# Optimization experiments

Measured on AMD Instinct MI355X. Metric: run time of the kernel, lower is better.

The kernel has to match this reference:

```python
import jax, jax.numpy as jnp
import numpy as np

N_NODES = 100000
N_EDGES = 1600000
N_PAIRS = 500000
IN_C, HID_C, OUT_C = 128, 128, 128


def setup_inputs() -> dict:
    key = jax.random.key(0)
    ks = jax.random.split(key, 12)
    def lin(k, fan_in, shape):
        b = 1.0 / np.sqrt(fan_in)
        return jax.random.uniform(k, shape, jnp.float32, -b, b)
    return {
        "x": jax.random.normal(ks[0], (N_NODES, IN_C), jnp.float32),
        "edge_index": jax.random.randint(ks[1], (2, N_EDGES), 0, N_NODES),
        "edge_pairs": jax.random.randint(ks[2], (2, N_PAIRS), 0, N_NODES),
        "W1": lin(ks[3], IN_C, (IN_C, HID_C)),
        "b1": jnp.zeros((HID_C,), jnp.float32),
        "W2": lin(ks[4], HID_C, (HID_C, OUT_C)),
        "b2": jnp.zeros((OUT_C,), jnp.float32),
        "Wm1": lin(ks[5], 2 * OUT_C, (2 * OUT_C, HID_C)),
        "bm1": lin(ks[6], 2 * OUT_C, (HID_C,)),
        "Wm2": lin(ks[7], HID_C, (HID_C, 1)),
        "bm2": lin(ks[8], HID_C, (1,)),
    }


def reference(x, edge_index, edge_pairs, W1, b1, W2, b2, Wm1, bm1, Wm2, bm2):
    N = x.shape[0]
    loop = jnp.arange(N, dtype=edge_index.dtype)
    row = jnp.concatenate([edge_index[0], loop])  # source nodes (+self loops)
    col = jnp.concatenate([edge_index[1], loop])  # target nodes (+self loops)
    # symmetric GCN normalization: deg^{-1/2}[row] * deg^{-1/2}[col]
    deg = jax.ops.segment_sum(jnp.ones(col.shape, x.dtype), col, num_segments=N)
    dinv = jnp.where(deg > 0, jax.lax.rsqrt(deg), 0.0)
    norm = dinv[row] * dinv[col]  # [E+N]

    def gcn_conv(h, W, b):
        h = h @ W  # transform first (PyG GCNConv lin has no bias)
        msg = h[row] * norm[:, None]
        return jax.ops.segment_sum(msg, col, num_segments=N) + b

    h = jax.nn.relu(gcn_conv(x, W1, b1))
    h = gcn_conv(h, W2, b2)  # dropout p=0.0 -> identity

    src, dst = edge_pairs[0], edge_pairs[1]
    ef = jnp.concatenate([h[src], h[dst]], axis=-1)  # [P, 2*out]
    out = jax.nn.relu(ef @ Wm1 + bm1) @ Wm2 + bm2
    return out.squeeze(-1)
```

## Files before the change

### kernel.cpp

```cpp
#include <hip/hip_runtime.h>
#include <hip/hip_fp16.h>

#define NCH 128
#define G_NODES 256
#define EPB 4096
#define RCAP 4864
#define MAXNB 512
#define KST 40

typedef __attribute__((ext_vector_type(8))) short short8;
typedef _Float16 half8 __attribute__((ext_vector_type(8)));
typedef __attribute__((ext_vector_type(4))) float floatx4;

static inline size_t align256(size_t x){ return (x + 255) & ~(size_t)255; }

__global__ __launch_bounds__(256) void wprep2_kernel(
    const float* __restrict__ W2, const float* __restrict__ Wm1,
    const float* __restrict__ b2, const float* __restrict__ bm1,
    short* __restrict__ planes, float* __restrict__ bm1p, float* __restrict__ zbias){
  int b = blockIdx.x, t = threadIdx.x;
  if (b == 128){
    if (t < 128){
      float acc = bm1[t];
      for (int j = 0; j < 128; j++)
        acc += b2[j] * (Wm1[j * 128 + t] + Wm1[(128 + j) * 128 + t]);
      bm1p[t] = acc;
      zbias[t] = 0.f;
    }
    return;
  }
  __shared__ float w2row[128];
  if (t < 128) w2row[t] = W2[b * 128 + t];
  __syncthreads();
  int mat = t >> 7, n = t & 127;
  const float* Wsrc = Wm1 + (size_t)mat * 16384;
  float acc = 0.f;
  #pragma unroll 4
  for (int j = 0; j < 128; j++) acc = fmaf(w2row[j], Wsrc[j * 128 + n], acc);
  __half h = __float2half(acc);
  __half l = __float2half(acc - __half2float(h));
  planes[(size_t)(4 + 2 * mat) * 16384 + n * 128 + b] = __half_as_short(h);
  planes[(size_t)(5 + 2 * mat) * 16384 + n * 128 + b] = __half_as_short(l);
}

__global__ __launch_bounds__(256) void binA_kernel(
    const int* __restrict__ row, const int* __restrict__ col,
    int* __restrict__ gcur, unsigned* __restrict__ bucketed, int E, int NB,
    const float* __restrict__ W1, short* __restrict__ planes){
  __shared__ int cnt[MAXNB];
  __shared__ int lbase[MAXNB];
  __shared__ int gbase[MAXNB];
  __shared__ unsigned sorted[EPB];
  __shared__ unsigned short binOf[EPB];
  __shared__ int sh[256];
  __shared__ int carry;
  int t = threadIdx.x;
  int e0 = blockIdx.x * EPB;
  int ecnt = min(EPB, E - e0);
  for (int i = t; i < NB; i += 256) cnt[i] = 0;
  if (t == 0) carry = 0;
  __syncthreads();
  unsigned rec[16]; int bn[16]; int rk[16];
  #pragma unroll
  for (int i = 0; i < 16; i++){
    int e = e0 + i * 256 + t;
    if (e < E){
      int r = row[e], c = col[e];
      bn[i]  = c >> 8;
      rec[i] = (unsigned)r | ((unsigned)(c & 255) << 17);
      rk[i]  = atomicAdd(&cnt[bn[i]], 1);
    } else bn[i] = -1;
  }
  __syncthreads();
  for (int start = 0; start < NB; start += 256){
    int i = start + t;
    int v = (i < NB) ? cnt[i] : 0;
    sh[t] = v; __syncthreads();
    for (int off = 1; off < 256; off <<= 1){
      int val = (t >= off) ? sh[t - off] : 0;
      __syncthreads(); sh[t] += val; __syncthreads();
    }
    if (i < NB) lbase[i] = sh[t] - v + carry;
    __syncthreads();
    if (t == 255) carry += sh[255];
    __syncthreads();
  }
  for (int i = t; i < NB; i += 256){
    int c = cnt[i];
    gbase[i] = (c > 0) ? atomicAdd(&gcur[i], c) : 0;
  }
  __syncthreads();
  #pragma unroll
  for (int i = 0; i < 16; i++){
    if (bn[i] >= 0){
      int pos = lbase[bn[i]] + rk[i];
      sorted[pos] = rec[i];
      binOf[pos]  = (unsigned short)bn[i];
    }
  }
  __syncthreads();
  for (int idx = t; idx < ecnt; idx += 256){
    int b = binOf[idx];
    int gpos = gbase[b] + (idx - lbase[b]);
    if (gpos < RCAP) bucketed[(size_t)b * RCAP + gpos] = sorted[idx];
  }
  {
    int gid = blockIdx.x * 256 + t;
    if (gid < 16384){
      int k = gid >> 7, n = gid & 127;
      float x = W1[gid];
      unsigned u = __float_as_uint(x);
      short hs = (short)(u >> 16);
      float hf = __uint_as_float(u & 0xFFFF0000u);
      short ls = (short)(__float_as_uint(x - hf) >> 16);
      planes[n * 128 + k]         = hs;
      planes[16384 + n * 128 + k] = ls;
    }
  }
}

__global__ __launch_bounds__(512, 4) void fused_gemm_binB(
    const float* __restrict__ X, const short* __restrict__ Whi_,
    const short* __restrict__ Wlo_, __half* __restrict__ O, int nrows, int gemmBlocks,
    const unsigned* __restrict__ bucketed, const int* __restrict__ gcur,
    int* __restrict__ rows_sorted, int* __restrict__ offs,
    int* __restrict__ counts, float* __restrict__ dinv, int N){
  __shared__ __align__(16) char smem[40960];
  int t = threadIdx.x;
  if (blockIdx.x < gemmBlocks){
    short* Xhi = (short*)smem;
    short* Xlo = Xhi + 128 * KST;
    short* Whi = Xlo + 128 * KST;
    short* Wlo = Whi + 128 * KST;
    int w = t >> 6, lane = t & 63;
    int m = lane & 15, q = lane >> 4;
    int row0 = blockIdx.x * 128;
    floatx4 acc[8];
    #pragma unroll
    for (int ct = 0; ct < 8; ct++) acc[ct] = (floatx4)0.f;
    for (int kc = 0; kc < 4; kc++){
      int k0 = kc * 32;
      __syncthreads();
      #pragma unroll
      for (int qq = 0; qq < 2; qq++){
        int f = t + 512 * qq;
        int r = f >> 3, kq = f & 7;
        int gr = row0 + r;
        int grc = (gr < nrows) ? gr : 0;
        float4 v = *(const float4*)(X + (size_t)grc * NCH + k0 + kq * 4);
        short h[4], l[4];
        float vv[4] = {v.x, v.y, v.z, v.w};
        #pragma unroll
        for (int j = 0; j < 4; j++){
          unsigned u = __float_as_uint(vv[j]);
          h[j] = (short)(u >> 16);
          float hf = __uint_as_float(u & 0xFFFF0000u);
          l[j] = (short)(__float_as_uint(vv[j] - hf) >> 16);
        }
        *(uint2*)(Xhi + r * KST + kq * 4) = *(uint2*)h;
        *(uint2*)(Xlo + r * KST + kq * 4) = *(uint2*)l;
      }
      {
        int n = t >> 2, kq = t & 3;
        *(uint4*)(Whi + n * KST + kq * 8) = *(const uint4*)(Whi_ + n * NCH + k0 + kq * 8);
        *(uint4*)(Wlo + n * KST + kq * 8) = *(const uint4*)(Wlo_ + n * NCH + k0 + kq * 8);
      }
      __syncthreads();
      short8 a_hi = *(const short8*)(Xhi + (w * 16 + m) * KST + q * 8);
      short8 a_lo = *(const short8*)(Xlo + (w * 16 + m) * KST + q * 8);
      #pragma unroll
      for (int ct = 0; ct < 8; ct++){
        short8 b_hi = *(const short8*)(Whi + (ct * 16 + m) * KST + q * 8);
        short8 b_lo = *(const short8*)(Wlo + (ct * 16 + m) * KST + q * 8);
        acc[ct] = __builtin_amdgcn_mfma_f32_16x16x32_bf16(a_hi, b_hi, acc[ct], 0, 0, 0);
        acc[ct] = __builtin_amdgcn_mfma_f32_16x16x32_bf16(a_lo, b_hi, acc[ct], 0, 0, 0);
        acc[ct] = __builtin_amdgcn_mfma_f32_16x16x32_bf16(a_hi, b_lo, acc[ct], 0, 0, 0);
      }
    }
    #pragma unroll
    for (int r = 0; r < 4; r++){
      int grow = row0 + w * 16 + q * 4 + r;
      if (grow < nrows){
        #pragma unroll
        for (int ct = 0; ct < 8; ct++)
          O[(size_t)grow * NCH + ct * 16 + m] = __float2half(acc[ct][r]);
      }
    }
  } else {
    int b = blockIdx.x - gemmBlocks;
    unsigned* ledge = (unsigned*)smem;
    int* cnt  = (int*)(smem + RCAP * 4);
    int* cnt2 = cnt + 256;
    int* lex  = cnt2 + 256;
    int* sh   = lex + 256;
    int size = min(gcur[b], RCAP);
    int n0 = b * G_NODES;
    if (t < 256){ cnt[t] = 0; cnt2[t] = 0; }
    __syncthreads();
    for (int i = t; i < size; i += 512){
      unsigned v = bucketed[(size_t)b * RCAP + i];
      ledge[i] = v;
      atomicAdd(&cnt[v >> 17], 1);
    }
    __syncthreads();
    {
      int v = (t < 256) ? cnt[t] : 0;
      if (t < 256) sh[t] = v;
      __syncthreads();
      for (int off = 1; off < 256; off <<= 1){
        int val = (t >= off && t < 256) ? sh[t - off] : 0;
        __syncthreads();
        if (t < 256) sh[t] += val;
        __syncthreads();
      }
      if (t < 256){
        lex[t] = sh[t] - v;
        int n = n0 + t;
        if (n < N){
          counts[n] = v;
          offs[n]   = b * RCAP + sh[t] - v;
          dinv[n]   = rsqrtf((float)v + 1.0f);
        }
      }
    }
    __syncthreads();
    for (int i = t; i < size; i += 512){
      unsigned v = ledge[i];
      int node = v >> 17;
      int pos = lex[node] + atomicAdd(&cnt2[node], 1);
      rows_sorted[(size_t)b * RCAP + pos] = (int)(v & 0x1FFFFu);
    }
  }
}

template<int NCT>
__global__ __launch_bounds__(512, 4) void gemm_f16k(
    const __half* __restrict__ X,
    const short* __restrict__ Whi0, const short* __restrict__ Wlo0,
    const short* __restrict__ Whi1, const short* __restrict__ Wlo1,
    const float* __restrict__ scale, int do_scale,
    __half* __restrict__ O0, __half* __restrict__ O1, int nrows){
  __shared__ short Xs[128 * KST];
  __shared__ short Whs[NCT * 16 * KST];
  __shared__ short Wls[NCT * 16 * KST];
  int t = threadIdx.x;
  int w = t >> 6, lane = t & 63;
  int m = lane & 15, q = lane >> 4;
  int row0 = blockIdx.x * 128;
  floatx4 acc[NCT];
  #pragma unroll
  for (int ct = 0; ct < NCT; ct++) acc[ct] = (floatx4)0.f;

  for (int kc = 0; kc < 4; kc++){
    int k0 = kc * 32;
    __syncthreads();
    {
      int r = t >> 2, kq = t & 3;
      int gr = row0 + r;
      int grc = (gr < nrows) ? gr : 0;
      *(uint4*)(Xs + r * KST + kq * 8) = *(const uint4*)(X + (size_t)grc * NCH + k0 + kq * 8);
    }
    #pragma unroll
    for (int i = t; i < NCT * 16 * 4; i += 512){
      int n = i >> 2, kq = i & 3;
      const short* sh = (n < 128) ? (Whi0 + n * NCH) : (Whi1 + (n - 128) * NCH);
      const short* sl = (n < 128) ? (Wlo0 + n * NCH) : (Wlo1 + (n - 128) * NCH);
      *(uint4*)(Whs + n * KST + kq * 8) = *(const uint4*)(sh + k0 + kq * 8);
      *(uint4*)(Wls + n * KST + kq * 8) = *(const uint4*)(sl + k0 + kq * 8);
    }
    __syncthreads();
    half8 a = *(const half8*)(Xs + (w * 16 + m) * KST + q * 8);
    #pragma unroll
    for (int ct = 0; ct < NCT; ct++){
      half8 bh = *(const half8*)(Whs + (ct * 16 + m) * KST + q * 8);
      half8 bl = *(const half8*)(Wls + (ct * 16 + m) * KST + q * 8);
      acc[ct] = __builtin_amdgcn_mfma_f32_16x16x32_f16(a, bh, acc[ct], 0, 0, 0);
      acc[ct] = __builtin_amdgcn_mfma_f32_16x16x32_f16(a, bl, acc[ct], 0, 0, 0);
    }
  }
  #pragma unroll
  for (int r = 0; r < 4; r++){
    int grow = row0 + w * 16 + q * 4 + r;
    if (grow < nrows){
      float sc = do_scale ? scale[grow] : 1.0f;
      #pragma unroll
      for (int ct = 0; ct < NCT; ct++){
        __half val = __float2half(acc[ct][r] * sc);
        if (ct < 8) O0[(size_t)grow * NCH + ct * 16 + m] = val;
        else        O1[(size_t)grow * NCH + (ct - 8) * 16 + m] = val;
      }
    }
  }
}

__global__ __launch_bounds__(256) void agg_kernel(
    const __half* __restrict__ s, const float* __restrict__ dinv,
    const int* __restrict__ offs, const int* __restrict__ counts,
    const int* __restrict__ rows_sorted, const float* __restrict__ bias,
    __half* __restrict__ outp, int N, int do_relu, int edge_dinv){
  int wave = (int)((blockIdx.x * blockDim.x + threadIdx.x) >> 6);
  int lane = threadIdx.x & 63;
  if (wave >= N) return;
  int c = wave;
  int g = lane >> 4, h = lane & 15;
  float di = dinv[c];
  float wself = edge_dinv ? di : 1.0f;
  float acc[8] = {0.f,0.f,0.f,0.f,0.f,0.f,0.f,0.f};
  if (g == 0){
    uint4 v = *(const uint4*)(s + (size_t)c * NCH + h * 8);
    const __half2* hp = (const __half2*)&v;
    #pragma unroll
    for (int i = 0; i < 4; i++){
      float2 f = __half22float2(hp[i]);
      acc[2*i] = fmaf(wself, f.x, acc[2*i]); acc[2*i+1] = fmaf(wself, f.y, acc[2*i+1]);
    }
  }
  int off = offs[c], cnt = counts[c];
  for (int chunk = 0; chunk < cnt; chunk += 64){
    int nn = min(64, cnt - chunk);
    int myidx = (lane < nn) ? rows_sorted[off + chunk + lane] : 0;
    float mydinv = 1.0f;
    if (edge_dinv && lane < nn) mydinv = dinv[myidx];
    int jmax = (nn + 3) >> 2;
    #pragma unroll 8
    for (int j = 0; j < jmax; j++){
      int e = 4 * j + g;
      int r  = __shfl(myidx, e & 63, 64);
      float dr = edge_dinv ? __shfl(mydinv, e & 63, 64) : 1.0f;
      if (e < nn){
        uint4 v = *(const uint4*)(s + (size_t)r * NCH + h * 8);
        const __half2* hp = (const __half2*)&v;
        #pragma unroll
        for (int i = 0; i < 4; i++){
          float2 f = __half22float2(hp[i]);
          acc[2*i] = fmaf(dr, f.x, acc[2*i]); acc[2*i+1] = fmaf(dr, f.y, acc[2*i+1]);
        }
      }
    }
  }
  #pragma unroll
  for (int i = 0; i < 8; i++){
    acc[i] += __shfl_xor(acc[i], 16, 64);
    acc[i] += __shfl_xor(acc[i], 32, 64);
  }
  if (g == 0){
    float4 b0 = *(const float4*)(bias + h * 8);
    float4 b1 = *(const float4*)(bias + h * 8 + 4);
    float o[8];
    o[0] = di*acc[0]+b0.x; o[1] = di*acc[1]+b0.y; o[2] = di*acc[2]+b0.z; o[3] = di*acc[3]+b0.w;
    o[4] = di*acc[4]+b1.x; o[5] = di*acc[5]+b1.y; o[6] = di*acc[6]+b1.z; o[7] = di*acc[7]+b1.w;
    if (do_relu){
      #pragma unroll
      for (int i = 0; i < 8; i++) o[i] = fmaxf(o[i], 0.f);
    }
    __half2 packed[4];
    #pragma unroll
    for (int i = 0; i < 4; i++) packed[i] = __floats2half2_rn(o[2*i], o[2*i+1]);
    *(uint4*)(outp + (size_t)c * NCH + h * 8) = *(uint4*)packed;
  }
}

__global__ __launch_bounds__(256) void pair_kernel(
    const __half* __restrict__ A, const __half* __restrict__ B,
    const int* __restrict__ src, const int* __restrict__ dst,
    const float* __restrict__ bm1, const float* __restrict__ Wm2,
    const float* __restrict__ bm2, float* __restrict__ outp, int P){
  int gwave = (int)((blockIdx.x * blockDim.x + threadIdx.x) >> 6);
  int lane  = threadIdx.x & 63;
  int nw    = (int)((gridDim.x * blockDim.x) >> 6);
  int g = lane >> 4, h = lane & 15;
  float bb[8], ww[8];
  {
    float4 t0 = *(const float4*)(bm1 + h * 8);
    float4 t1 = *(const float4*)(bm1 + h * 8 + 4);
    bb[0]=t0.x; bb[1]=t0.y; bb[2]=t0.z; bb[3]=t0.w;
    bb[4]=t1.x; bb[5]=t1.y; bb[6]=t1.z; bb[7]=t1.w;
    float4 w0 = *(const float4*)(Wm2 + h * 8);
    float4 w1 = *(const float4*)(Wm2 + h * 8 + 4);
    ww[0]=w0.x; ww[1]=w0.y; ww[2]=w0.z; ww[3]=w0.w;
    ww[4]=w1.x; ww[5]=w1.y; ww[6]=w1.z; ww[7]=w1.w;
  }
  float bsc = bm2[0];
  const __half* basep = (g & 1) ? B : A;
  const int* idxp = (g & 1) ? dst : src;
  for (int p0 = gwave * 8; p0 < P; p0 += nw * 8){
    int piA = p0 + (g >> 1);
    int piB = p0 + 2 + (g >> 1);
    int piC = p0 + 4 + (g >> 1);
    int piD = p0 + 6 + (g >> 1);
    int piAX = (piA < P) ? piA : P - 1;
    int piBX = (piB < P) ? piB : P - 1;
    int piCX = (piC < P) ? piC : P - 1;
    int piDX = (piD < P) ? piD : P - 1;
    int nodeA = idxp[piAX];
    int nodeB = idxp[piBX];
    int nodeC = idxp[piCX];
    int nodeD = idxp[piDX];
    uint4 vA = *(const uint4*)(basep + (size_t)nodeA * NCH + h * 8);
    uint4 vB = *(const uint4*)(basep + (size_t)nodeB * NCH + h * 8);
    uint4 vC = *(const uint4*)(basep + (size_t)nodeC * NCH + h * 8);
    uint4 vD = *(const uint4*)(basep + (size_t)nodeD * NCH + h * 8);
    const __half2* hpA = (const __half2*)&vA;
    const __half2* hpB = (const __half2*)&vB;
    const __half2* hpC = (const __half2*)&vC;
    const __half2* hpD = (const __half2*)&vD;
    float fA[8], fB[8], fC[8], fD[8];
    #pragma unroll
    for (int i = 0; i < 4; i++){
      float2 ta = __half22float2(hpA[i]);
      float2 tb = __half22float2(hpB[i]);
      float2 tc = __half22float2(hpC[i]);
      float2 td = __half22float2(hpD[i]);
      fA[2*i] = ta.x; fA[2*i+1] = ta.y;
      fB[2*i] = tb.x; fB[2*i+1] = tb.y;
      fC[2*i] = tc.x; fC[2*i+1] = tc.y;
      fD[2*i] = td.x; fD[2*i+1] = td.y;
    }
    float pA = 0.f, pB = 0.f, pC = 0.f, pD = 0.f;
    #pragma unroll
    for (int i = 0; i < 8; i++){
      float oA = __shfl_xor(fA[i], 16, 64);
      float oB = __shfl_xor(fB[i], 16, 64);
      float oC = __shfl_xor(fC[i], 16, 64);
      float oD = __shfl_xor(fD[i], 16, 64);
      float zA = fmaxf(fA[i] + oA + bb[i], 0.f);
      float zB = fmaxf(fB[i] + oB + bb[i], 0.f);
      float zC = fmaxf(fC[i] + oC + bb[i], 0.f);
      float zD = fmaxf(fD[i] + oD + bb[i], 0.f);
      pA += zA * ww[i];
      pB += zB * ww[i];
      pC += zC * ww[i];
      pD += zD * ww[i];
    }
    #pragma unroll
    for (int d = 1; d <= 8; d <<= 1){
      pA += __shfl_xor(pA, d, 64);
      pB += __shfl_xor(pB, d, 64);
      pC += __shfl_xor(pC, d, 64);
      pD += __shfl_xor(pD, d, 64);
    }
    if ((lane & 31) == 0){
      if (piA < P) outp[piA] = pA + bsc;
      if (piB < P) outp[piB] = pB + bsc;
      if (piC < P) outp[piC] = pC + bsc;
      if (piD < P) outp[piD] = pD + bsc;
    }
  }
}


extern "C" void kernel_launch(void* const* d_in, const int* in_sizes, int n_in,
                              void* d_out, int out_size, void* d_ws, size_t ws_size,
                              hipStream_t stream){
  const float* x   = (const float*)d_in[0];
  const int*   ei  = (const int*)  d_in[1];
  const int*   ep  = (const int*)  d_in[2];
  const float* W1  = (const float*)d_in[3];
  const float* b1  = (const float*)d_in[4];
  const float* W2  = (const float*)d_in[5];
  const float* b2  = (const float*)d_in[6];
  const float* Wm1 = (const float*)d_in[7];
  const float* bm1 = (const float*)d_in[8];
  const float* Wm2 = (const float*)d_in[9];
  const float* bm2 = (const float*)d_in[10];
  float* outp = (float*)d_out;

  const int N = in_sizes[0] / NCH;
  const int E = in_sizes[1] / 2;
  const int P = in_sizes[2] / 2;
  const int NB = (N + G_NODES - 1) / G_NODES;

  char* base = (char*)d_ws;
  size_t off = 0;
  int*      counts      = (int*)     (base + off); off = align256(off + (size_t)N * 4);
  int*      offs        = (int*)     (base + off); off = align256(off + (size_t)N * 4);
  float*    dinv        = (float*)   (base + off); off = align256(off + (size_t)N * 4);
  int*      gcur        = (int*)     (base + off); off = align256(off + (size_t)NB * 4);
  unsigned* bucketed    = (unsigned*)(base + off); off = align256(off + (size_t)NB * RCAP * 4);
  int*      rows_sorted = (int*)     (base + off); off = align256(off + (size_t)NB * RCAP * 4);
  short*    planes      = (short*)   (base + off); off = align256(off + (size_t)8 * 16384 * 2);
  float*    bm1p        = (float*)   (base + off); off = align256(off + (size_t)256 * 4);
  float*    zbias       = (float*)   (base + off); off = align256(off + (size_t)128 * 4);
  __half*   s1buf       = (__half*)  (base + off); off = align256(off + (size_t)N * NCH * 2);
  __half*   h1buf       = (__half*)  (base + off); off = align256(off + (size_t)N * NCH * 2);
  __half*   zbuf        = (__half*)  (base + off); off = align256(off + (size_t)N * NCH * 2);
  __half*   sA          = (__half*)  (base + off); off = align256(off + (size_t)N * NCH * 2);
  __half*   sB          = (__half*)  (base + off); off = align256(off + (size_t)N * NCH * 2);
  (void)ws_size; (void)n_in; (void)out_size;

  short* W1hi = planes + 0 * 16384;
  short* W1lo = planes + 1 * 16384;
  short* Wahi = planes + 4 * 16384;
  short* Walo = planes + 5 * 16384;
  short* Wbhi = planes + 6 * 16384;
  short* Wblo = planes + 7 * 16384;

  const int* row = ei;
  const int* col = ei + E;
  const int* psrc = ep;
  const int* pdst = ep + P;

  int gemm_grid = (N + 127) / 128;
  int agg_grid  = (N + 3) / 4;

  wprep2_kernel<<<129, 256, 0, stream>>>(W2, Wm1, b2, bm1, planes, bm1p, zbias);
  hipMemsetAsync(gcur, 0, (size_t)NB * 4, stream);
  binA_kernel<<<(E + EPB - 1) / EPB, 256, 0, stream>>>(row, col, gcur, bucketed, E, NB,
                                                       W1, planes);
  fused_gemm_binB<<<gemm_grid + NB, 512, 0, stream>>>(
      x, W1hi, W1lo, s1buf, N, gemm_grid,
      bucketed, gcur, rows_sorted, offs, counts, dinv, N);
  agg_kernel<<<agg_grid, 256, 0, stream>>>(s1buf, dinv, offs, counts, rows_sorted, b1, h1buf, N, 1, 1);
  agg_kernel<<<agg_grid, 256, 0, stream>>>(h1buf, dinv, offs, counts, rows_sorted, zbias, zbuf, N, 0, 1);
  gemm_f16k<16><<<gemm_grid, 512, 0, stream>>>(zbuf, Wahi, Walo, Wbhi, Wblo, dinv, 0, sA, sB, N);
  pair_kernel<<<8192, 256, 0, stream>>>(sA, sB, psrc, pdst, bm1p, Wm2, bm2, outp, P);
}
```

Measured before the change: 374.9 us.

## Fold weight-prep into binning kernel and deepen pair-kernel load batching

Removes the separate wprep2 launch by folding the W2·Wm1 plane precompute and bias fold into extra blocks of binA_kernel, enlarging its grid to at least 193 blocks. The pair kernel now issues eight independent gathers per lane per iteration instead of four, to expose more memory-level parallelism on the random row gathers. This saves one launch and its serialization, but adds register pressure in the pair kernel. It also adds a __syncthreads inside a block-index branch of binA; this is uniform per block, so it is safe.

```diff
diff --git a/kernel.cpp b/kernel.cpp
--- a/kernel.cpp
+++ b/kernel.cpp
@@ -14,39 +14,13 @@
 
 static inline size_t align256(size_t x){ return (x + 255) & ~(size_t)255; }
 
-__global__ __launch_bounds__(256) void wprep2_kernel(
-    const float* __restrict__ W2, const float* __restrict__ Wm1,
-    const float* __restrict__ b2, const float* __restrict__ bm1,
-    short* __restrict__ planes, float* __restrict__ bm1p, float* __restrict__ zbias){
-  int b = blockIdx.x, t = threadIdx.x;
-  if (b == 128){
-    if (t < 128){
-      float acc = bm1[t];
-      for (int j = 0; j < 128; j++)
-        acc += b2[j] * (Wm1[j * 128 + t] + Wm1[(128 + j) * 128 + t]);
-      bm1p[t] = acc;
-      zbias[t] = 0.f;
-    }
-    return;
-  }
-  __shared__ float w2row[128];
-  if (t < 128) w2row[t] = W2[b * 128 + t];
-  __syncthreads();
-  int mat = t >> 7, n = t & 127;
-  const float* Wsrc = Wm1 + (size_t)mat * 16384;
-  float acc = 0.f;
-  #pragma unroll 4
-  for (int j = 0; j < 128; j++) acc = fmaf(w2row[j], Wsrc[j * 128 + n], acc);
-  __half h = __float2half(acc);
-  __half l = __float2half(acc - __half2float(h));
-  planes[(size_t)(4 + 2 * mat) * 16384 + n * 128 + b] = __half_as_short(h);
-  planes[(size_t)(5 + 2 * mat) * 16384 + n * 128 + b] = __half_as_short(l);
-}
-
 __global__ __launch_bounds__(256) void binA_kernel(
     const int* __restrict__ row, const int* __restrict__ col,
     int* __restrict__ gcur, unsigned* __restrict__ bucketed, int E, int NB,
-    const float* __restrict__ W1, short* __restrict__ planes){
+    const float* __restrict__ W1, const float* __restrict__ W2,
+    const float* __restrict__ Wm1, const float* __restrict__ b2,
+    const float* __restrict__ bm1, short* __restrict__ planes,
+    float* __restrict__ bm1p, float* __restrict__ zbias){
   __shared__ int cnt[MAXNB];
   __shared__ int lbase[MAXNB];
   __shared__ int gbase[MAXNB];
@@ -54,6 +28,7 @@
   __shared__ unsigned short binOf[EPB];
   __shared__ int sh[256];
   __shared__ int carry;
+  __shared__ float w2row[128];
   int t = threadIdx.x;
   int e0 = blockIdx.x * EPB;
   int ecnt = min(EPB, E - e0);
@@ -115,6 +90,28 @@
       short ls = (short)(__float_as_uint(x - hf) >> 16);
       planes[n * 128 + k]         = hs;
       planes[16384 + n * 128 + k] = ls;
+    }
+  }
+  if (blockIdx.x >= 64 && blockIdx.x < 192){
+    int b = blockIdx.x - 64;
+    if (t < 128) w2row[t] = W2[b * 128 + t];
+    __syncthreads();
+    int mat = t >> 7, n = t & 127;
+    const float* Wsrc = Wm1 + (size_t)mat * 16384;
+    float acc = 0.f;
+    #pragma unroll 4
+    for (int j = 0; j < 128; j++) acc = fmaf(w2row[j], Wsrc[j * 128 + n], acc);
+    __half hh = __float2half(acc);
+    __half ll = __float2half(acc - __half2float(hh));
+    planes[(size_t)(4 + 2 * mat) * 16384 + n * 128 + b] = __half_as_short(hh);
+    planes[(size_t)(5 + 2 * mat) * 16384 + n * 128 + b] = __half_as_short(ll);
+  } else if (blockIdx.x == 192){
+    if (t < 128){
+      float acc = bm1[t];
+      for (int j = 0; j < 128; j++)
+        acc += b2[j] * (Wm1[j * 128 + t] + Wm1[(128 + j) * 128 + t]);
+      bm1p[t] = acc;
+      zbias[t] = 0.f;
     }
   }
 }
@@ -383,67 +380,44 @@
   float bsc = bm2[0];
   const __half* basep = (g & 1) ? B : A;
   const int* idxp = (g & 1) ? dst : src;
-  for (int p0 = gwave * 8; p0 < P; p0 += nw * 8){
-    int piA = p0 + (g >> 1);
-    int piB = p0 + 2 + (g >> 1);
-    int piC = p0 + 4 + (g >> 1);
-    int piD = p0 + 6 + (g >> 1);
-    int piAX = (piA < P) ? piA : P - 1;
-    int piBX = (piB < P) ? piB : P - 1;
-    int piCX = (piC < P) ? piC : P - 1;
-    int piDX = (piD < P) ? piD : P - 1;
-    int nodeA = idxp[piAX];
-    int nodeB = idxp[piBX];
-    int nodeC = idxp[piCX];
-    int nodeD = idxp[piDX];
-    uint4 vA = *(const uint4*)(basep + (size_t)nodeA * NCH + h * 8);
-    uint4 vB = *(const uint4*)(basep + (size_t)nodeB * NCH + h * 8);
-    uint4 vC = *(const uint4*)(basep + (size_t)nodeC * NCH + h * 8);
-    uint4 vD = *(const uint4*)(basep + (size_t)nodeD * NCH + h * 8);
-    const __half2* hpA = (const __half2*)&vA;
-    const __half2* hpB = (const __half2*)&vB;
-    const __half2* hpC = (const __half2*)&vC;
-    const __half2* hpD = (const __half2*)&vD;
-    float fA[8], fB[8], fC[8], fD[8];
-    #pragma unroll
-    for (int i = 0; i < 4; i++){
-      float2 ta = __half22float2(hpA[i]);
-      float2 tb = __half22float2(hpB[i]);
-      float2 tc = __half22float2(hpC[i]);
-      float2 td = __half22float2(hpD[i]);
-      fA[2*i] = ta.x; fA[2*i+1] = ta.y;
-      fB[2*i] = tb.x; fB[2*i+1] = tb.y;
-      fC[2*i] = tc.x; fC[2*i+1] = tc.y;
-      fD[2*i] = td.x; fD[2*i+1] = td.y;
-    }
-    float pA = 0.f, pB = 0.f, pC = 0.f, pD = 0.f;
-    #pragma unroll
-    for (int i = 0; i < 8; i++){
-      float oA = __shfl_xor(fA[i], 16, 64);
-      float oB = __shfl_xor(fB[i], 16, 64);
-      float oC = __shfl_xor(fC[i], 16, 64);
-      float oD = __shfl_xor(fD[i], 16, 64);
-      float zA = fmaxf(fA[i] + oA + bb[i], 0.f);
-      float zB = fmaxf(fB[i] + oB + bb[i], 0.f);
-      float zC = fmaxf(fC[i] + oC + bb[i], 0.f);
-      float zD = fmaxf(fD[i] + oD + bb[i], 0.f);
-      pA += zA * ww[i];
-      pB += zB * ww[i];
-      pC += zC * ww[i];
-      pD += zD * ww[i];
-    }
-    #pragma unroll
-    for (int d = 1; d <= 8; d <<= 1){
-      pA += __shfl_xor(pA, d, 64);
-      pB += __shfl_xor(pB, d, 64);
-      pC += __shfl_xor(pC, d, 64);
-      pD += __shfl_xor(pD, d, 64);
+  int s = g >> 1;
+  for (int p0 = gwave * 16; p0 < P; p0 += nw * 16){
+    int pi[8]; uint4 v[8];
+    #pragma unroll
+    for (int k = 0; k < 8; k++){
+      int p = p0 + 2 * k + s;
+      pi[k] = p;
+      int px = (p < P) ? p : P - 1;
+      int node = idxp[px];
+      v[k] = *(const uint4*)(basep + (size_t)node * NCH + h * 8);
+    }
+    float pr[8];
+    #pragma unroll
+    for (int k = 0; k < 8; k++){
+      const __half2* hp = (const __half2*)&v[k];
+      float f[8];
+      #pragma unroll
+      for (int i = 0; i < 4; i++){
+        float2 t2 = __half22float2(hp[i]);
+        f[2*i] = t2.x; f[2*i+1] = t2.y;
+      }
+      float p_ = 0.f;
+      #pragma unroll
+      for (int i = 0; i < 8; i++){
+        float o = __shfl_xor(f[i], 16, 64);
+        p_ += fmaxf(f[i] + o + bb[i], 0.f) * ww[i];
+      }
+      pr[k] = p_;
+    }
+    #pragma unroll
+    for (int k = 0; k < 8; k++){
+      #pragma unroll
+      for (int d = 1; d <= 8; d <<= 1) pr[k] += __shfl_xor(pr[k], d, 64);
     }
     if ((lane & 31) == 0){
-      if (piA < P) outp[piA] = pA + bsc;
-      if (piB < P) outp[piB] = pB + bsc;
-      if (piC < P) outp[piC] = pC + bsc;
-      if (piD < P) outp[piD] = pD + bsc;
+      #pragma unroll
+      for (int k = 0; k < 8; k++)
+        if (pi[k] < P) outp[pi[k]] = pr[k] + bsc;
     }
   }
 }
@@ -502,11 +476,12 @@
 
   int gemm_grid = (N + 127) / 128;
   int agg_grid  = (N + 3) / 4;
-
-  wprep2_kernel<<<129, 256, 0, stream>>>(W2, Wm1, b2, bm1, planes, bm1p, zbias);
+  int binA_grid = (E + EPB - 1) / EPB;
+  if (binA_grid < 193) binA_grid = 193;
+
   hipMemsetAsync(gcur, 0, (size_t)NB * 4, stream);
-  binA_kernel<<<(E + EPB - 1) / EPB, 256, 0, stream>>>(row, col, gcur, bucketed, E, NB,
-                                                       W1, planes);
+  binA_kernel<<<binA_grid, 256, 0, stream>>>(row, col, gcur, bucketed, E, NB,
+                                             W1, W2, Wm1, b2, bm1, planes, bm1p, zbias);
   fused_gemm_binB<<<gemm_grid + NB, 512, 0, stream>>>(
       x, W1hi, W1lo, s1buf, N, gemm_grid,
       bucketed, gcur, rows_sorted, offs, counts, dinv, N);
```

Result: no change. 371.5 us, median of 2 (-0.9%).
